# Kernel tuning notes

Hardware: AMD Instinct MI355X
Metric: run time of the kernel (lower is better)

The kernel has to match this reference:

```python
import jax, jax.numpy as jnp
import numpy as np

# ---- static config (mirrors init_kwargs) ----
EMBED_DIM = 128
NUM_HEADS = 4
N_SUB = 16       # token grid is N_SUB x N_SUB, seq = N_SUB**2
WINDOW = 4
SHIFT = 2
EPS = 1e-5
NEG_INF = -1e9


def _swin_mask(n_sub, ws, shift):
    """Standard Swin attention mask for shifted windows. [NW, T, T]."""
    img = np.zeros((n_sub, n_sub), np.int32)
    cnt = 0
    for hs in (slice(0, -ws), slice(-ws, -shift), slice(-shift, None)):
        for wsl in (slice(0, -ws), slice(-ws, -shift), slice(-shift, None)):
            img[hs, wsl] = cnt
            cnt += 1
    nw = n_sub // ws
    ids = img.reshape(nw, ws, nw, ws).transpose(0, 2, 1, 3).reshape(nw * nw, ws * ws)
    mask = np.where(ids[:, None, :] != ids[:, :, None], NEG_INF, 0.0).astype(np.float32)
    return jnp.asarray(mask)


MASK = _swin_mask(N_SUB, WINDOW, SHIFT)


def _inorm(v):
    # InstanceNorm2d (affine=False) over spatial dims, per (batch, seq, channel)
    m = v.mean(axis=(-2, -1), keepdims=True)
    var = v.var(axis=(-2, -1), keepdims=True)
    return (v - m) * jax.lax.rsqrt(var + EPS)


def _pw(x, w, b):
    # pointwise (1x1) linear over channel dim of [..., C, H, W]
    return jnp.einsum('...chw,cd->...dhw', x, w) + b[:, None, None]


def _window(x, nw, ws):
    # [B, n_sub, n_sub, C, H, W] -> [B, nw*nw, ws*ws, C, H, W]
    B = x.shape[0]
    C, H, W = x.shape[3:]
    x = x.reshape(B, nw, ws, nw, ws, C, H, W)
    return x.transpose(0, 1, 3, 2, 4, 5, 6, 7).reshape(B, nw * nw, ws * ws, C, H, W)


def _unwindow(x, nw, ws):
    B = x.shape[0]
    C, H, W = x.shape[3:]
    x = x.reshape(B, nw, nw, ws, ws, C, H, W)
    return x.transpose(0, 1, 3, 2, 4, 5, 6, 7).reshape(B, nw * ws, nw * ws, C, H, W)


def _swin_func_attn(v, w_q, b_q, w_k, b_k, w_v, b_v, w_o, b_o):
    B, S, C, H, W = v.shape
    nw = N_SUB // WINDOW
    g = v.reshape(B, N_SUB, N_SUB, C, H, W)
    if SHIFT > 0:
        g = jnp.roll(g, (-SHIFT, -SHIFT), axis=(1, 2))
    q = _window(_pw(g, w_q, b_q), nw, WINDOW)
    k = _window(_pw(g, w_k, b_k), nw, WINDOW)
    val = _window(_pw(g, w_v, b_v), nw, WINDOW)
    d = C // NUM_HEADS
    T = WINDOW * WINDOW
    split = lambda x: x.reshape(B, nw * nw, T, NUM_HEADS, d, H, W)
    q, k, val = split(q), split(k), split(val)
    # integral score: spatial mean of per-head dot products, scaled by sqrt(d)
    scale = 1.0 / (np.sqrt(d) * H * W)
    scores = jnp.einsum('bnthdxy,bnshdxy->bnhts', q, k) * scale
    scores = scores + MASK[None, :, None, :, :]
    attn = jax.nn.softmax(scores, axis=-1)
    o = jnp.einsum('bnhts,bnshdxy->bnthdxy', attn, val)
    o = o.reshape(B, nw * nw, T, C, H, W)
    o = _pw(o, w_o, b_o)
    o = _unwindow(o, nw, WINDOW)
    if SHIFT > 0:
        o = jnp.roll(o, (SHIFT, SHIFT), axis=(1, 2))
    return o.reshape(B, S, C, H, W)


def _mlp(x, w1, b1, w2, b2):
    return _pw(jax.nn.gelu(_pw(x, w1, b1)), w2, b2)


def setup_inputs() -> dict:
    key = jax.random.key(0)
    ks = jax.random.split(key, 8)
    B, S, C, H, W = 8, N_SUB * N_SUB, EMBED_DIM, 16, 16
    p = 0.02
    return {
        'v': jax.random.normal(ks[0], (B, S, C, H, W), jnp.float32),
        'w_q': jax.random.normal(ks[1], (C, C), jnp.float32) * p,
        'b_q': jnp.zeros((C,), jnp.float32),
        'w_k': jax.random.normal(ks[2], (C, C), jnp.float32) * p,
        'b_k': jnp.zeros((C,), jnp.float32),
        'w_v': jax.random.normal(ks[3], (C, C), jnp.float32) * p,
        'b_v': jnp.zeros((C,), jnp.float32),
        'w_o': jax.random.normal(ks[4], (C, C), jnp.float32) * p,
        'b_o': jnp.zeros((C,), jnp.float32),
        'w1': jax.random.normal(ks[5], (C, C), jnp.float32) * p,
        'b1': jnp.zeros((C,), jnp.float32),
        'w2': jax.random.normal(ks[6], (C, C), jnp.float32) * p,
        'b2': jnp.zeros((C,), jnp.float32),
    }


def reference(v, w_q, b_q, w_k, b_k, w_v, b_v, w_o, b_o, w1, b1, w2, b2):
    v = _swin_func_attn(_inorm(v), w_q, b_q, w_k, b_k, w_v, b_v, w_o, b_o) + v
    v = _mlp(_inorm(v), w1, b1, w2, b2) + v
    return v
```

## Files before the change

kernel.cpp:

```cpp
#include <hip/hip_runtime.h>
#include <cstdint>
#include <cstddef>

#define DI __device__ __forceinline__

typedef unsigned short u16;
typedef u16 u16x8 __attribute__((ext_vector_type(8)));
typedef u16 u16x4 __attribute__((ext_vector_type(4)));
typedef float f32x4 __attribute__((ext_vector_type(4)));
typedef __bf16 bf16x8 __attribute__((ext_vector_type(8)));

constexpr float EPSf  = 1e-5f;
constexpr float SCALE = 1.0f / (5.656854249492381f * 256.0f);

DI float bf2f(u16 u) { union { uint32_t i; float f; } v; v.i = ((uint32_t)u) << 16; return v.f; }
DI u16 f2bf(float f) {
    union { float f; uint32_t i; } v; v.f = f;
    uint32_t r = v.i + 0x7fffu + ((v.i >> 16) & 1u);
    return (u16)(r >> 16);
}

DI f32x4 MFMA(bf16x8 a, bf16x8 b, f32x4 c) {
    return __builtin_amdgcn_mfma_f32_16x16x32_bf16(a, b, c, 0, 0, 0);
}

DI int region3(int x) { return x < 12 ? 0 : (x < 14 ? 1 : 2); }

DI float gelu_f(float x) {
    float u = 1.5957691216f * x * (1.f + 0.044715f * x * x);
    return x * __builtin_amdgcn_rcpf(1.f + __expf(-u));
}

__global__ __launch_bounds__(256) void kw_prep(
        const float* __restrict__ w_q, const float* __restrict__ w_k,
        const float* __restrict__ w_v, const float* __restrict__ w_o,
        const float* __restrict__ w1,  const float* __restrict__ w2,
        u16* __restrict__ wt) {
    __shared__ float lds[128 * 129];
    const float* W;
    switch (blockIdx.x) {
        case 0: W = w_q; break; case 1: W = w_k; break; case 2: W = w_v; break;
        case 3: W = w_o; break; case 4: W = w1;  break; default: W = w2;  break;
    }
    u16* O = wt + blockIdx.x * 16384;
    int tid = threadIdx.x;
    for (int i = 0; i < 16; i++) {
        int flat = i * 1024 + tid * 4;
        float4 vv = *(const float4*)(W + flat);
        int c = flat >> 7, d = flat & 127;
        lds[c * 129 + d + 0] = vv.x; lds[c * 129 + d + 1] = vv.y;
        lds[c * 129 + d + 2] = vv.z; lds[c * 129 + d + 3] = vv.w;
    }
    __syncthreads();
    for (int i = 0; i < 32; i++) {
        int flat2 = i * 512 + tid * 2;
        int d = flat2 >> 7, c = flat2 & 127;
        u16 a = f2bf(lds[c * 129 + d]);
        u16 b = f2bf(lds[(c + 1) * 129 + d]);
        uint32_t pk = (uint32_t)a | ((uint32_t)b << 16);
        *(uint32_t*)(O + flat2) = pk;
    }
}

__global__ __launch_bounds__(512) void k2_qkv(
        const float* __restrict__ v, const u16* __restrict__ wt,
        const float* __restrict__ b_q, const float* __restrict__ b_k,
        const float* __restrict__ b_v,
        u16* __restrict__ Qg, u16* __restrict__ Kg, u16* __restrict__ Vg) {
    __shared__ u16 Abuf[256 * 136];
    __shared__ float red[2][4][128];
    __shared__ float stats[2][128];

    int tid = threadIdx.x;
    int wtk = blockIdx.x;
    int b = wtk >> 8, n = (wtk >> 4) & 15, t = wtk & 15;
    int wi = n >> 2, wj = n & 3, ti = t >> 2, tj = t & 3;
    int si = (wi * 4 + ti + 2) & 15, sj = (wj * 4 + tj + 2) & 15;
    const float* src = v + (size_t)(b * 256 + si * 16 + sj) * 32768;

    int xy = tid & 255, chh = tid >> 8;
    #pragma unroll 4
    for (int g = 0; g < 16; g++) {
        int c0 = chh * 64 + g * 4;
        float x0 = src[(c0 + 0) * 256 + xy];
        float x1 = src[(c0 + 1) * 256 + xy];
        float x2 = src[(c0 + 2) * 256 + xy];
        float x3 = src[(c0 + 3) * 256 + xy];
        u16x4 u; u.x = f2bf(x0); u.y = f2bf(x1); u.z = f2bf(x2); u.w = f2bf(x3);
        *(u16x4*)&Abuf[xy * 136 + c0] = u;
    }
    __syncthreads();
    {
        int c = tid & 127, p = tid >> 7;
        float s = 0.f, q = 0.f;
        for (int k = 0; k < 64; k++) {
            float x = bf2f(Abuf[(p * 64 + k) * 136 + c]);
            s += x; q += x * x;
        }
        red[0][p][c] = s; red[1][p][c] = q;
    }
    __syncthreads();
    if (tid < 128) {
        int c = tid;
        float s = red[0][0][c] + red[0][1][c] + red[0][2][c] + red[0][3][c];
        float q = red[1][0][c] + red[1][1][c] + red[1][2][c] + red[1][3][c];
        float mean = s * (1.f / 256.f);
        float var = q * (1.f / 256.f) - mean * mean;
        stats[0][c] = mean; stats[1][c] = rsqrtf(var + EPSf);
    }
    __syncthreads();
    for (int g = 0; g < 16; g++) {
        int c0 = chh * 64 + g * 4;
        u16x4 u = *(u16x4*)&Abuf[xy * 136 + c0];
        u.x = f2bf((bf2f(u.x) - stats[0][c0 + 0]) * stats[1][c0 + 0]);
        u.y = f2bf((bf2f(u.y) - stats[0][c0 + 1]) * stats[1][c0 + 1]);
        u.z = f2bf((bf2f(u.z) - stats[0][c0 + 2]) * stats[1][c0 + 2]);
        u.w = f2bf((bf2f(u.w) - stats[0][c0 + 3]) * stats[1][c0 + 3]);
        *(u16x4*)&Abuf[xy * 136 + c0] = u;
    }
    __syncthreads();

    int wave = tid >> 6, lane = tid & 63;
    int lrow = lane & 15, quad = lane >> 4;
    bf16x8 afr[2][4];
    for (int mi = 0; mi < 2; mi++) {
        int mt = wave * 2 + mi;
        for (int kt = 0; kt < 4; kt++)
            afr[mi][kt] = *(const bf16x8*)&Abuf[(mt * 16 + lrow) * 136 + kt * 32 + quad * 8];
    }
    __syncthreads();
    u16* WTs  = Abuf;
    u16* stgw = Abuf + 17408 + wave * 2176;
    for (int w = 0; w < 3; w++) {
        const u16* WTp = wt + w * 16384;
        const float* bias = (w == 0) ? b_q : (w == 1) ? b_k : b_v;
        u16* O = ((w == 0) ? Qg : (w == 1) ? Kg : Vg) + (size_t)wtk * 32768;
        if (w) __syncthreads();
        for (int i = 0; i < 4; i++) {
            int flat = i * 4096 + tid * 8;
            *(u16x8*)&WTs[(flat >> 7) * 136 + (flat & 127)] =
                *(const u16x8*)&WTp[flat];
        }
        __syncthreads();
        f32x4 acc[2][8];
        for (int mi = 0; mi < 2; mi++)
            for (int nt = 0; nt < 8; nt++) acc[mi][nt] = (f32x4){0.f, 0.f, 0.f, 0.f};
        for (int kt = 0; kt < 4; kt++) {
            for (int nt = 0; nt < 8; nt++) {
                bf16x8 bfr = *(const bf16x8*)&WTs[(nt * 16 + lrow) * 136 + kt * 32 + quad * 8];
                acc[0][nt] = MFMA(afr[0][kt], bfr, acc[0][nt]);
                acc[1][nt] = MFMA(afr[1][kt], bfr, acc[1][nt]);
            }
        }
        for (int mi = 0; mi < 2; mi++) {
            int mt = wave * 2 + mi;
            for (int nt = 0; nt < 8; nt++) {
                int d = nt * 16 + lrow;
                float bv = bias[d];
                for (int r = 0; r < 4; r++)
                    stgw[(quad * 4 + r) * 136 + d] = f2bf(acc[mi][nt][r] + bv);
            }
            for (int ro = 0; ro < 4; ro++) {
                int flat = ro * 512 + lane * 8;
                *(u16x8*)&O[mt * 2048 + flat] =
                    *(const u16x8*)&stgw[(flat >> 7) * 136 + (flat & 127)];
            }
        }
    }
}

__global__ __launch_bounds__(1024, 4) void k3_scores(
        const u16* __restrict__ Qg, const u16* __restrict__ Kg,
        float* __restrict__ spart) {
    __shared__ f32x4 red3[3][4][64];
    int tid = threadIdx.x;
    int bid = blockIdx.x;
    int b = bid >> 5, n = (bid >> 1) & 15, half = bid & 1;
    int wtb = (b * 16 + n) * 16;
    int lane = tid & 63, wave = tid >> 6;
    int head = wave & 3, sub = wave >> 2;
    int lrow = lane & 15, quad = lane >> 4;
    int xyb = half * 128 + sub * 32;
    const u16* Qp = Qg + (size_t)(wtb + lrow) * 32768 + (size_t)xyb * 128 + head * 32 + quad * 8;
    const u16* Kp = Kg + (size_t)(wtb + lrow) * 32768 + (size_t)xyb * 128 + head * 32 + quad * 8;
    f32x4 acc = {0.f, 0.f, 0.f, 0.f};
    #pragma unroll 4
    for (int kt = 0; kt < 32; kt++) {
        bf16x8 aq = *(const bf16x8*)(Qp + kt * 128);
        bf16x8 bk = *(const bf16x8*)(Kp + kt * 128);
        acc = MFMA(aq, bk, acc);
    }
    if (sub) red3[sub - 1][head][lane] = acc;
    __syncthreads();
    if (sub == 0) {
        f32x4 a0 = red3[0][head][lane];
        f32x4 a1 = red3[1][head][lane];
        f32x4 a2 = red3[2][head][lane];
        acc = acc + a0 + a1 + a2;
        float* sp = spart + (size_t)(((half * 8 + b) * 16 + n) * 4 + head) * 256;
        for (int r = 0; r < 4; r++) sp[(quad * 4 + r) * 16 + lrow] = acc[r];
    }
}

__global__ __launch_bounds__(512) void k4_attnout(
        const float* __restrict__ v, const u16* __restrict__ Vg,
        const float* __restrict__ spart, const u16* __restrict__ wt,
        const float* __restrict__ b_o, u16* __restrict__ v2) {
    __shared__ u16 Vc[32768];
    __shared__ u16 Obuf[256 * 136];
    __shared__ float attn[4][16][16];
    int tid = threadIdx.x;
    int bid = blockIdx.x;
    int b = bid >> 6, n = (bid >> 2) & 15, qtr = bid & 3;
    int wi = n >> 2, wj = n & 3;
    int wtb = (b * 16 + n) * 16;

    if (tid < 64) {
        int h = tid >> 4, t = tid & 15;
        int it = wi * 4 + (t >> 2) , jt = wj * 4 + (t & 3);
        int rt = region3(it) * 3 + region3(jt);
        const float* sp0 = spart + (size_t)(((0 + b) * 16 + n) * 4 + h) * 256 + t * 16;
        const float* sp1 = spart + (size_t)(((8 + b) * 16 + n) * 4 + h) * 256 + t * 16;
        float vals[16]; float mx = -1e30f;
        for (int s = 0; s < 16; s++) {
            int is = wi * 4 + (s >> 2), js = wj * 4 + (s & 3);
            int rs = region3(is) * 3 + region3(js);
            float sc = (sp0[s] + sp1[s]) * SCALE + (rs == rt ? 0.f : -1e9f);
            vals[s] = sc; mx = fmaxf(mx, sc);
        }
        float sum = 0.f;
        for (int s = 0; s < 16; s++) { vals[s] = __expf(vals[s] - mx); sum += vals[s]; }
        float inv = 1.f / sum;
        for (int s = 0; s < 16; s++) attn[h][t][s] = vals[s] * inv;
    }
    __syncthreads();

    int lane = tid & 63, wave = tid >> 6;
    int lrow = lane & 15, quad = lane >> 4;
    const u16* WoT = wt + 3 * 16384;

    for (int sub = 0; sub < 4; sub++) {
        int xyb = qtr * 64 + sub * 16;
        if (sub) __syncthreads();
        for (int it = 0; it < 8; it++) {
            int flat = (it * 512 + tid) * 8;
            int s = flat >> 11, rem = flat & 2047;
            *(u16x8*)&Vc[flat] =
                *(const u16x8*)&Vg[(size_t)(wtb + s) * 32768 + xyb * 128 + rem];
        }
        __syncthreads();
        {
            int c = tid & 127, xg = tid >> 7;
            int h = c >> 5;
            float vreg[4][16];
            for (int rep = 0; rep < 4; rep++) {
                int xyl = xg * 4 + rep;
                for (int s = 0; s < 16; s++)
                    vreg[rep][s] = bf2f(Vc[s * 2048 + xyl * 128 + c]);
            }
            for (int t = 0; t < 16; t++) {
                float oa0 = 0.f, oa1 = 0.f, oa2 = 0.f, oa3 = 0.f;
                for (int s = 0; s < 16; s++) {
                    float a = attn[h][t][s];
                    oa0 += a * vreg[0][s]; oa1 += a * vreg[1][s];
                    oa2 += a * vreg[2][s]; oa3 += a * vreg[3][s];
                }
                Obuf[(t * 16 + xg * 4 + 0) * 136 + c] = f2bf(oa0);
                Obuf[(t * 16 + xg * 4 + 1) * 136 + c] = f2bf(oa1);
                Obuf[(t * 16 + xg * 4 + 2) * 136 + c] = f2bf(oa2);
                Obuf[(t * 16 + xg * 4 + 3) * 136 + c] = f2bf(oa3);
            }
        }
        __syncthreads();
        bf16x8 afr[2][4];
        for (int mi = 0; mi < 2; mi++) {
            int mt = wave * 2 + mi;
            for (int kt = 0; kt < 4; kt++)
                afr[mi][kt] = *(const bf16x8*)&Obuf[(mt * 16 + lrow) * 136 + kt * 32 + quad * 8];
        }
        f32x4 acc[2][8];
        for (int mi = 0; mi < 2; mi++)
            for (int nt = 0; nt < 8; nt++) acc[mi][nt] = (f32x4){0.f, 0.f, 0.f, 0.f};
        for (int kt = 0; kt < 4; kt++) {
            for (int nt = 0; nt < 8; nt++) {
                bf16x8 bfr = *(const bf16x8*)&WoT[(nt * 16 + lrow) * 128 + kt * 32 + quad * 8];
                acc[0][nt] = MFMA(afr[0][kt], bfr, acc[0][nt]);
                acc[1][nt] = MFMA(afr[1][kt], bfr, acc[1][nt]);
            }
        }
        u16* stgw = Vc + wave * 2176;
        for (int mi = 0; mi < 2; mi++) {
            int mt = wave * 2 + mi;
            int sd = (((wi * 4 + (mt >> 2) + 2) & 15) << 4) | ((wj * 4 + (mt & 3) + 2) & 15);
            size_t tokbase = (size_t)(b * 256 + sd) * 32768;
            for (int nt = 0; nt < 8; nt++) {
                int c = nt * 16 + lrow;
                float bv = b_o[c];
                float4 res = *(const float4*)&v[tokbase + (size_t)c * 256 + xyb + quad * 4];
                stgw[(quad * 4 + 0) * 136 + c] = f2bf(acc[mi][nt][0] + bv + res.x);
                stgw[(quad * 4 + 1) * 136 + c] = f2bf(acc[mi][nt][1] + bv + res.y);
                stgw[(quad * 4 + 2) * 136 + c] = f2bf(acc[mi][nt][2] + bv + res.z);
                stgw[(quad * 4 + 3) * 136 + c] = f2bf(acc[mi][nt][3] + bv + res.w);
            }
            size_t obase = tokbase + (size_t)xyb * 128;
            for (int ro = 0; ro < 4; ro++) {
                int flat = ro * 512 + lane * 8;
                *(u16x8*)&v2[obase + flat] =
                    *(const u16x8*)&stgw[(flat >> 7) * 136 + (flat & 127)];
            }
        }
    }
}

__global__ __launch_bounds__(512) void k6_mlp(
        const u16* __restrict__ v2, const u16* __restrict__ wt,
        const float* __restrict__ b1, const float* __restrict__ b2,
        float* __restrict__ out) {
    __shared__ u16 Nbuf[256 * 136];
    __shared__ u16 Hbuf[256 * 136];
    __shared__ float red[2][4][128];
    __shared__ float stats[3][128];
    int tid = threadIdx.x;
    size_t tok = blockIdx.x;
    const u16* src = v2 + tok * 32768;

    for (int it = 0; it < 8; it++) {
        int flat = (it * 512 + tid) * 8;
        int xy = flat >> 7, c = flat & 127;
        *(u16x8*)&Nbuf[xy * 136 + c] = *(const u16x8*)&src[flat];
    }
    __syncthreads();
    {
        int c = tid & 127, p = tid >> 7;
        float s = 0.f, q = 0.f;
        for (int k = 0; k < 64; k++) {
            float x = bf2f(Nbuf[(p * 64 + k) * 136 + c]);
            s += x; q += x * x;
        }
        red[0][p][c] = s; red[1][p][c] = q;
    }
    __syncthreads();
    if (tid < 128) {
        int c = tid;
        float s = red[0][0][c] + red[0][1][c] + red[0][2][c] + red[0][3][c];
        float q = red[1][0][c] + red[1][1][c] + red[1][2][c] + red[1][3][c];
        float mean = s * (1.f / 256.f);
        float var = q * (1.f / 256.f) - mean * mean;
        float rstd = rsqrtf(var + EPSf);
        stats[0][c] = mean; stats[1][c] = rstd; stats[2][c] = (var + EPSf) * rstd;
    }
    __syncthreads();
    {
        int c0 = (tid & 31) * 4, xyB = tid >> 5;
        for (int g = 0; g < 16; g++) {
            int xy = g * 16 + xyB;
            u16x4 u = *(u16x4*)&Nbuf[xy * 136 + c0];
            u.x = f2bf((bf2f(u.x) - stats[0][c0 + 0]) * stats[1][c0 + 0]);
            u.y = f2bf((bf2f(u.y) - stats[0][c0 + 1]) * stats[1][c0 + 1]);
            u.z = f2bf((bf2f(u.z) - stats[0][c0 + 2]) * stats[1][c0 + 2]);
            u.w = f2bf((bf2f(u.w) - stats[0][c0 + 3]) * stats[1][c0 + 3]);
            *(u16x4*)&Nbuf[xy * 136 + c0] = u;
        }
    }
    {
        const u16* W1T = wt + 4 * 16384;
        for (int i = 0; i < 4; i++) {
            int flat = i * 4096 + tid * 8;
            *(u16x8*)&Hbuf[(flat >> 7) * 136 + (flat & 127)] = *(const u16x8*)&W1T[flat];
        }
    }
    __syncthreads();

    int wave = tid >> 6, lane = tid & 63;
    int lrow = lane & 15, quad = lane >> 4;
    const u16* W2T = wt + 5 * 16384;

    {
        bf16x8 afr[2][4];
        for (int mi = 0; mi < 2; mi++) {
            int mt = wave * 2 + mi;
            for (int kt = 0; kt < 4; kt++)
                afr[mi][kt] = *(const bf16x8*)&Nbuf[(mt * 16 + lrow) * 136 + kt * 32 + quad * 8];
        }
        f32x4 acc[2][8];
        for (int mi = 0; mi < 2; mi++)
            for (int nt = 0; nt < 8; nt++) acc[mi][nt] = (f32x4){0.f, 0.f, 0.f, 0.f};
        for (int kt = 0; kt < 4; kt++) {
            for (int nt = 0; nt < 8; nt++) {
                bf16x8 bfr = *(const bf16x8*)&Hbuf[(nt * 16 + lrow) * 136 + kt * 32 + quad * 8];
                acc[0][nt] = MFMA(afr[0][kt], bfr, acc[0][nt]);
                acc[1][nt] = MFMA(afr[1][kt], bfr, acc[1][nt]);
            }
        }
        __syncthreads();
        for (int mi = 0; mi < 2; mi++) {
            int mt = wave * 2 + mi;
            for (int nt = 0; nt < 8; nt++) {
                int c = nt * 16 + lrow;
                float bv = b1[c];
                for (int r = 0; r < 4; r++) {
                    float x = acc[mi][nt][r] + bv;
                    Hbuf[(mt * 16 + quad * 4 + r) * 136 + c] = f2bf(gelu_f(x));
                }
            }
        }
    }
    {
        bf16x8 afr[2][4];
        for (int mi = 0; mi < 2; mi++) {
            int mt = wave * 2 + mi;
            for (int kt = 0; kt < 4; kt++)
                afr[mi][kt] = *(const bf16x8*)&Hbuf[(mt * 16 + lrow) * 136 + kt * 32 + quad * 8];
        }
        f32x4 acc[2][8];
        for (int mi = 0; mi < 2; mi++)
            for (int nt = 0; nt < 8; nt++) acc[mi][nt] = (f32x4){0.f, 0.f, 0.f, 0.f};
        for (int kt = 0; kt < 4; kt++) {
            for (int nt = 0; nt < 8; nt++) {
                bf16x8 bfr = *(const bf16x8*)&W2T[(nt * 16 + lrow) * 128 + kt * 32 + quad * 8];
                acc[0][nt] = MFMA(afr[0][kt], bfr, acc[0][nt]);
                acc[1][nt] = MFMA(afr[1][kt], bfr, acc[1][nt]);
            }
        }
        for (int mi = 0; mi < 2; mi++) {
            int mt = wave * 2 + mi;
            for (int nt = 0; nt < 8; nt++) {
                int c = nt * 16 + lrow;
                float mean = stats[0][c], sd = stats[2][c], bv = b2[c];
                f32x4 o4;
                for (int r = 0; r < 4; r++) {
                    int m = mt * 16 + quad * 4 + r;
                    float n2v = bf2f(Nbuf[m * 136 + c]);
                    o4[r] = acc[mi][nt][r] + bv + n2v * sd + mean;
                }
                *(f32x4*)&out[tok * 32768 + (size_t)c * 256 + mt * 16 + quad * 4] = o4;
            }
        }
    }
}

extern "C" void kernel_launch(void* const* d_in, const int* in_sizes, int n_in,
                              void* d_out, int out_size, void* d_ws, size_t ws_size,
                              hipStream_t stream) {
    const float* v   = (const float*)d_in[0];
    const float* w_q = (const float*)d_in[1];
    const float* b_q = (const float*)d_in[2];
    const float* w_k = (const float*)d_in[3];
    const float* b_k = (const float*)d_in[4];
    const float* w_v = (const float*)d_in[5];
    const float* b_v = (const float*)d_in[6];
    const float* w_o = (const float*)d_in[7];
    const float* b_o = (const float*)d_in[8];
    const float* w1  = (const float*)d_in[9];
    const float* b1  = (const float*)d_in[10];
    const float* w2  = (const float*)d_in[11];
    const float* b2  = (const float*)d_in[12];

    u16*   wt    = (u16*)d_ws;
    float* spart = (float*)((char*)d_ws + 196608);
    u16*   Qg    = (u16*)((char*)d_ws + 1245184);
    u16*   v2    = Qg;
    u16*   Vg    = (u16*)d_out;
    u16*   Kg    = (u16*)d_out + 67108864;
    float* out   = (float*)d_out;

    kw_prep  <<<6,    256,  0, stream>>>(w_q, w_k, w_v, w_o, w1, w2, wt);
    k2_qkv   <<<2048, 512,  0, stream>>>(v, wt, b_q, b_k, b_v, Qg, Kg, Vg);
    k3_scores<<<256,  1024, 0, stream>>>(Qg, Kg, spart);
    k4_attnout<<<512, 512,  0, stream>>>(v, Vg, spart, wt, b_o, v2);
    k6_mlp   <<<2048, 512,  0, stream>>>(v2, wt, b1, b2, out);
}
```

Measured before the change: 1.042 ms.

## Double block size to 1024 threads in qkv, attnout and mlp kernels

Raises k2_qkv, k4_attnout and k6_mlp to 1024 threads so each wave owns one 16-row M tile instead of two. k2 now loads the input with float4 reads, computes the norm stats in registers and applies them as a single fmaf while transposing into LDS. k2 and k6 stop staging the weights in LDS and read the B fragments straight from global/L2. The aim is more waves in flight, fewer LDS passes and fewer barriers, at the cost of extra global weight reads and launch bounds that may force register spilling.

```diff
diff --git a/kernel.cpp b/kernel.cpp
--- a/kernel.cpp
+++ b/kernel.cpp
@@ -62,13 +62,13 @@
     }
 }
 
-__global__ __launch_bounds__(512) void k2_qkv(
+__global__ __launch_bounds__(1024, 4) void k2_qkv(
         const float* __restrict__ v, const u16* __restrict__ wt,
         const float* __restrict__ b_q, const float* __restrict__ b_k,
         const float* __restrict__ b_v,
         u16* __restrict__ Qg, u16* __restrict__ Kg, u16* __restrict__ Vg) {
-    __shared__ u16 Abuf[256 * 136];
-    __shared__ float red[2][4][128];
+    __shared__ __align__(16) u16 Abuf[256 * 136];
+    __shared__ float red[2][8][128];
     __shared__ float stats[2][128];
 
     int tid = threadIdx.x;
@@ -78,93 +78,72 @@
     int si = (wi * 4 + ti + 2) & 15, sj = (wj * 4 + tj + 2) & 15;
     const float* src = v + (size_t)(b * 256 + si * 16 + sj) * 32768;
 
-    int xy = tid & 255, chh = tid >> 8;
-    #pragma unroll 4
-    for (int g = 0; g < 16; g++) {
-        int c0 = chh * 64 + g * 4;
-        float x0 = src[(c0 + 0) * 256 + xy];
-        float x1 = src[(c0 + 1) * 256 + xy];
-        float x2 = src[(c0 + 2) * 256 + xy];
-        float x3 = src[(c0 + 3) * 256 + xy];
-        u16x4 u; u.x = f2bf(x0); u.y = f2bf(x1); u.z = f2bf(x2); u.w = f2bf(x3);
-        *(u16x4*)&Abuf[xy * 136 + c0] = u;
-    }
-    __syncthreads();
-    {
-        int c = tid & 127, p = tid >> 7;
-        float s = 0.f, q = 0.f;
-        for (int k = 0; k < 64; k++) {
-            float x = bf2f(Abuf[(p * 64 + k) * 136 + c]);
-            s += x; q += x * x;
-        }
-        red[0][p][c] = s; red[1][p][c] = q;
-    }
+    int c = tid & 127, xyq = tid >> 7;
+    float vals[32];
+    float s = 0.f, q = 0.f;
+    #pragma unroll
+    for (int g = 0; g < 8; g++) {
+        float4 f = *(const float4*)(src + c * 256 + g * 32 + xyq * 4);
+        vals[g * 4 + 0] = f.x; vals[g * 4 + 1] = f.y;
+        vals[g * 4 + 2] = f.z; vals[g * 4 + 3] = f.w;
+        s += f.x + f.y + f.z + f.w;
+        q += f.x * f.x + f.y * f.y + f.z * f.z + f.w * f.w;
+    }
+    red[0][xyq][c] = s; red[1][xyq][c] = q;
     __syncthreads();
     if (tid < 128) {
-        int c = tid;
-        float s = red[0][0][c] + red[0][1][c] + red[0][2][c] + red[0][3][c];
-        float q = red[1][0][c] + red[1][1][c] + red[1][2][c] + red[1][3][c];
-        float mean = s * (1.f / 256.f);
-        float var = q * (1.f / 256.f) - mean * mean;
-        stats[0][c] = mean; stats[1][c] = rsqrtf(var + EPSf);
-    }
-    __syncthreads();
-    for (int g = 0; g < 16; g++) {
-        int c0 = chh * 64 + g * 4;
-        u16x4 u = *(u16x4*)&Abuf[xy * 136 + c0];
-        u.x = f2bf((bf2f(u.x) - stats[0][c0 + 0]) * stats[1][c0 + 0]);
-        u.y = f2bf((bf2f(u.y) - stats[0][c0 + 1]) * stats[1][c0 + 1]);
-        u.z = f2bf((bf2f(u.z) - stats[0][c0 + 2]) * stats[1][c0 + 2]);
-        u.w = f2bf((bf2f(u.w) - stats[0][c0 + 3]) * stats[1][c0 + 3]);
-        *(u16x4*)&Abuf[xy * 136 + c0] = u;
-    }
+        float ss = 0.f, qq = 0.f;
+        #pragma unroll
+        for (int p = 0; p < 8; p++) { ss += red[0][p][tid]; qq += red[1][p][tid]; }
+        float mean = ss * (1.f / 256.f);
+        float var = qq * (1.f / 256.f) - mean * mean;
+        float a = rsqrtf(var + EPSf);
+        stats[0][tid] = a; stats[1][tid] = -mean * a;
+    }
+    __syncthreads();
+    float na = stats[0][c], nb = stats[1][c];
+    #pragma unroll
+    for (int g = 0; g < 8; g++)
+        #pragma unroll
+        for (int j = 0; j < 4; j++)
+            Abuf[(g * 32 + xyq * 4 + j) * 136 + c] = f2bf(fmaf(vals[g * 4 + j], na, nb));
     __syncthreads();
 
     int wave = tid >> 6, lane = tid & 63;
     int lrow = lane & 15, quad = lane >> 4;
-    bf16x8 afr[2][4];
-    for (int mi = 0; mi < 2; mi++) {
-        int mt = wave * 2 + mi;
-        for (int kt = 0; kt < 4; kt++)
-            afr[mi][kt] = *(const bf16x8*)&Abuf[(mt * 16 + lrow) * 136 + kt * 32 + quad * 8];
-    }
-    __syncthreads();
-    u16* WTs  = Abuf;
-    u16* stgw = Abuf + 17408 + wave * 2176;
+    bf16x8 afr[4];
+    #pragma unroll
+    for (int kt = 0; kt < 4; kt++)
+        afr[kt] = *(const bf16x8*)&Abuf[(wave * 16 + lrow) * 136 + kt * 32 + quad * 8];
+    u16* stgw = Abuf + wave * 2176;
     for (int w = 0; w < 3; w++) {
         const u16* WTp = wt + w * 16384;
         const float* bias = (w == 0) ? b_q : (w == 1) ? b_k : b_v;
         u16* O = ((w == 0) ? Qg : (w == 1) ? Kg : Vg) + (size_t)wtk * 32768;
-        if (w) __syncthreads();
-        for (int i = 0; i < 4; i++) {
-            int flat = i * 4096 + tid * 8;
-            *(u16x8*)&WTs[(flat >> 7) * 136 + (flat & 127)] =
-                *(const u16x8*)&WTp[flat];
-        }
-        __syncthreads();
-        f32x4 acc[2][8];
-        for (int mi = 0; mi < 2; mi++)
-            for (int nt = 0; nt < 8; nt++) acc[mi][nt] = (f32x4){0.f, 0.f, 0.f, 0.f};
+        f32x4 acc[8];
+        #pragma unroll
+        for (int nt = 0; nt < 8; nt++) acc[nt] = (f32x4){0.f, 0.f, 0.f, 0.f};
+        #pragma unroll
         for (int kt = 0; kt < 4; kt++) {
+            #pragma unroll
             for (int nt = 0; nt < 8; nt++) {
-                bf16x8 bfr = *(const bf16x8*)&WTs[(nt * 16 + lrow) * 136 + kt * 32 + quad * 8];
-                acc[0][nt] = MFMA(afr[0][kt], bfr, acc[0][nt]);
-                acc[1][nt] = MFMA(afr[1][kt], bfr, acc[1][nt]);
-            }
-        }
-        for (int mi = 0; mi < 2; mi++) {
-            int mt = wave * 2 + mi;
-            for (int nt = 0; nt < 8; nt++) {
-                int d = nt * 16 + lrow;
-                float bv = bias[d];
-                for (int r = 0; r < 4; r++)
-                    stgw[(quad * 4 + r) * 136 + d] = f2bf(acc[mi][nt][r] + bv);
-            }
-            for (int ro = 0; ro < 4; ro++) {
-                int flat = ro * 512 + lane * 8;
-                *(u16x8*)&O[mt * 2048 + flat] =
-                    *(const u16x8*)&stgw[(flat >> 7) * 136 + (flat & 127)];
-            }
+                bf16x8 bfr = *(const bf16x8*)&WTp[(nt * 16 + lrow) * 128 + kt * 32 + quad * 8];
+                acc[nt] = MFMA(afr[kt], bfr, acc[nt]);
+            }
+        }
+        #pragma unroll
+        for (int nt = 0; nt < 8; nt++) {
+            int d = nt * 16 + lrow;
+            float bv = bias[d];
+            #pragma unroll
+            for (int r = 0; r < 4; r++)
+                stgw[(quad * 4 + r) * 136 + d] = f2bf(acc[nt][r] + bv);
+        }
+        #pragma unroll
+        for (int ro = 0; ro < 4; ro++) {
+            int flat = ro * 512 + lane * 8;
+            *(u16x8*)&O[wave * 2048 + flat] =
+                *(const u16x8*)&stgw[(flat >> 7) * 136 + (flat & 127)];
         }
     }
 }
@@ -202,12 +181,12 @@
     }
 }
 
-__global__ __launch_bounds__(512) void k4_attnout(
+__global__ __launch_bounds__(1024, 4) void k4_attnout(
         const float* __restrict__ v, const u16* __restrict__ Vg,
         const float* __restrict__ spart, const u16* __restrict__ wt,
         const float* __restrict__ b_o, u16* __restrict__ v2) {
-    __shared__ u16 Vc[32768];
-    __shared__ u16 Obuf[256 * 136];
+    __shared__ __align__(16) u16 Vc[32768];
+    __shared__ __align__(16) u16 Obuf[256 * 136];
     __shared__ float attn[4][16][16];
     int tid = threadIdx.x;
     int bid = blockIdx.x;
@@ -242,8 +221,9 @@
     for (int sub = 0; sub < 4; sub++) {
         int xyb = qtr * 64 + sub * 16;
         if (sub) __syncthreads();
-        for (int it = 0; it < 8; it++) {
-            int flat = (it * 512 + tid) * 8;
+        #pragma unroll
+        for (int it = 0; it < 4; it++) {
+            int flat = (it * 1024 + tid) * 8;
             int s = flat >> 11, rem = flat & 2047;
             *(u16x8*)&Vc[flat] =
                 *(const u16x8*)&Vg[(size_t)(wtb + s) * 32768 + xyb * 128 + rem];
@@ -252,89 +232,92 @@
         {
             int c = tid & 127, xg = tid >> 7;
             int h = c >> 5;
-            float vreg[4][16];
-            for (int rep = 0; rep < 4; rep++) {
-                int xyl = xg * 4 + rep;
+            float vreg[2][16];
+            #pragma unroll
+            for (int rep = 0; rep < 2; rep++) {
+                int xyl = xg * 2 + rep;
+                #pragma unroll
                 for (int s = 0; s < 16; s++)
                     vreg[rep][s] = bf2f(Vc[s * 2048 + xyl * 128 + c]);
             }
+            #pragma unroll
             for (int t = 0; t < 16; t++) {
-                float oa0 = 0.f, oa1 = 0.f, oa2 = 0.f, oa3 = 0.f;
+                float oa0 = 0.f, oa1 = 0.f;
+                #pragma unroll
                 for (int s = 0; s < 16; s++) {
                     float a = attn[h][t][s];
                     oa0 += a * vreg[0][s]; oa1 += a * vreg[1][s];
-                    oa2 += a * vreg[2][s]; oa3 += a * vreg[3][s];
                 }
-                Obuf[(t * 16 + xg * 4 + 0) * 136 + c] = f2bf(oa0);
-                Obuf[(t * 16 + xg * 4 + 1) * 136 + c] = f2bf(oa1);
-                Obuf[(t * 16 + xg * 4 + 2) * 136 + c] = f2bf(oa2);
-                Obuf[(t * 16 + xg * 4 + 3) * 136 + c] = f2bf(oa3);
+                Obuf[(t * 16 + xg * 2 + 0) * 136 + c] = f2bf(oa0);
+                Obuf[(t * 16 + xg * 2 + 1) * 136 + c] = f2bf(oa1);
             }
         }
         __syncthreads();
-        bf16x8 afr[2][4];
-        for (int mi = 0; mi < 2; mi++) {
-            int mt = wave * 2 + mi;
-            for (int kt = 0; kt < 4; kt++)
-                afr[mi][kt] = *(const bf16x8*)&Obuf[(mt * 16 + lrow) * 136 + kt * 32 + quad * 8];
-        }
-        f32x4 acc[2][8];
-        for (int mi = 0; mi < 2; mi++)
-            for (int nt = 0; nt < 8; nt++) acc[mi][nt] = (f32x4){0.f, 0.f, 0.f, 0.f};
+        bf16x8 afr[4];
+        #pragma unroll
+        for (int kt = 0; kt < 4; kt++)
+            afr[kt] = *(const bf16x8*)&Obuf[(wave * 16 + lrow) * 136 + kt * 32 + quad * 8];
+        f32x4 acc[8];
+        #pragma unroll
+        for (int nt = 0; nt < 8; nt++) acc[nt] = (f32x4){0.f, 0.f, 0.f, 0.f};
+        #pragma unroll
         for (int kt = 0; kt < 4; kt++) {
+            #pragma unroll
             for (int nt = 0; nt < 8; nt++) {
                 bf16x8 bfr = *(const bf16x8*)&WoT[(nt * 16 + lrow) * 128 + kt * 32 + quad * 8];
-                acc[0][nt] = MFMA(afr[0][kt], bfr, acc[0][nt]);
-                acc[1][nt] = MFMA(afr[1][kt], bfr, acc[1][nt]);
-            }
-        }
-        u16* stgw = Vc + wave * 2176;
-        for (int mi = 0; mi < 2; mi++) {
-            int mt = wave * 2 + mi;
-            int sd = (((wi * 4 + (mt >> 2) + 2) & 15) << 4) | ((wj * 4 + (mt & 3) + 2) & 15);
-            size_t tokbase = (size_t)(b * 256 + sd) * 32768;
-            for (int nt = 0; nt < 8; nt++) {
-                int c = nt * 16 + lrow;
-                float bv = b_o[c];
-                float4 res = *(const float4*)&v[tokbase + (size_t)c * 256 + xyb + quad * 4];
-                stgw[(quad * 4 + 0) * 136 + c] = f2bf(acc[mi][nt][0] + bv + res.x);
-                stgw[(quad * 4 + 1) * 136 + c] = f2bf(acc[mi][nt][1] + bv + res.y);
-                stgw[(quad * 4 + 2) * 136 + c] = f2bf(acc[mi][nt][2] + bv + res.z);
-                stgw[(quad * 4 + 3) * 136 + c] = f2bf(acc[mi][nt][3] + bv + res.w);
-            }
-            size_t obase = tokbase + (size_t)xyb * 128;
-            for (int ro = 0; ro < 4; ro++) {
-                int flat = ro * 512 + lane * 8;
-                *(u16x8*)&v2[obase + flat] =
-                    *(const u16x8*)&stgw[(flat >> 7) * 136 + (flat & 127)];
-            }
-        }
-    }
-}
-
-__global__ __launch_bounds__(512) void k6_mlp(
+                acc[nt] = MFMA(afr[kt], bfr, acc[nt]);
+            }
+        }
+        int mt = wave;
+        int sd = (((wi * 4 + (mt >> 2) + 2) & 15) << 4) | ((wj * 4 + (mt & 3) + 2) & 15);
+        size_t tokbase = (size_t)(b * 256 + sd) * 32768;
+        u16* stgw = Obuf + wave * 2176;
+        #pragma unroll
+        for (int nt = 0; nt < 8; nt++) {
+            int cc = nt * 16 + lrow;
+            float bv = b_o[cc];
+            float4 res = *(const float4*)&v[tokbase + (size_t)cc * 256 + xyb + quad * 4];
+            stgw[(quad * 4 + 0) * 136 + cc] = f2bf(acc[nt][0] + bv + res.x);
+            stgw[(quad * 4 + 1) * 136 + cc] = f2bf(acc[nt][1] + bv + res.y);
+            stgw[(quad * 4 + 2) * 136 + cc] = f2bf(acc[nt][2] + bv + res.z);
+            stgw[(quad * 4 + 3) * 136 + cc] = f2bf(acc[nt][3] + bv + res.w);
+        }
+        size_t obase = tokbase + (size_t)xyb * 128;
+        #pragma unroll
+        for (int ro = 0; ro < 4; ro++) {
+            int flat = ro * 512 + lane * 8;
+            *(u16x8*)&v2[obase + flat] =
+                *(const u16x8*)&stgw[(flat >> 7) * 136 + (flat & 127)];
+        }
+    }
+}
+
+__global__ __launch_bounds__(1024, 4) void k6_mlp(
         const u16* __restrict__ v2, const u16* __restrict__ wt,
         const float* __restrict__ b1, const float* __restrict__ b2,
         float* __restrict__ out) {
-    __shared__ u16 Nbuf[256 * 136];
-    __shared__ u16 Hbuf[256 * 136];
-    __shared__ float red[2][4][128];
+    __shared__ __align__(16) u16 Nbuf[256 * 136];
+    __shared__ __align__(16) u16 Hbuf[256 * 136];
+    __shared__ float red[2][8][128];
     __shared__ float stats[3][128];
     int tid = threadIdx.x;
     size_t tok = blockIdx.x;
     const u16* src = v2 + tok * 32768;
 
-    for (int it = 0; it < 8; it++) {
-        int flat = (it * 512 + tid) * 8;
-        int xy = flat >> 7, c = flat & 127;
-        *(u16x8*)&Nbuf[xy * 136 + c] = *(const u16x8*)&src[flat];
+    u16x8 ld[4];
+    #pragma unroll
+    for (int it = 0; it < 4; it++) {
+        int flat = (it * 1024 + tid) * 8;
+        int xy = flat >> 7, cc = flat & 127;
+        ld[it] = *(const u16x8*)&src[flat];
+        *(u16x8*)&Nbuf[xy * 136 + cc] = ld[it];
     }
     __syncthreads();
     {
         int c = tid & 127, p = tid >> 7;
         float s = 0.f, q = 0.f;
-        for (int k = 0; k < 64; k++) {
-            float x = bf2f(Nbuf[(p * 64 + k) * 136 + c]);
+        for (int k = 0; k < 32; k++) {
+            float x = bf2f(Nbuf[(p * 32 + k) * 136 + c]);
             s += x; q += x * x;
         }
         red[0][p][c] = s; red[1][p][c] = q;
@@ -342,8 +325,9 @@
     __syncthreads();
     if (tid < 128) {
         int c = tid;
-        float s = red[0][0][c] + red[0][1][c] + red[0][2][c] + red[0][3][c];
-        float q = red[1][0][c] + red[1][1][c] + red[1][2][c] + red[1][3][c];
+        float s = 0.f, q = 0.f;
+        #pragma unroll
+        for (int p = 0; p < 8; p++) { s += red[0][p][c]; q += red[1][p][c]; }
         float mean = s * (1.f / 256.f);
         float var = q * (1.f / 256.f) - mean * mean;
         float rstd = rsqrtf(var + EPSf);
@@ -351,90 +335,87 @@
     }
     __syncthreads();
     {
-        int c0 = (tid & 31) * 4, xyB = tid >> 5;
-        for (int g = 0; g < 16; g++) {
-            int xy = g * 16 + xyB;
-            u16x4 u = *(u16x4*)&Nbuf[xy * 136 + c0];
-            u.x = f2bf((bf2f(u.x) - stats[0][c0 + 0]) * stats[1][c0 + 0]);
-            u.y = f2bf((bf2f(u.y) - stats[0][c0 + 1]) * stats[1][c0 + 1]);
-            u.z = f2bf((bf2f(u.z) - stats[0][c0 + 2]) * stats[1][c0 + 2]);
-            u.w = f2bf((bf2f(u.w) - stats[0][c0 + 3]) * stats[1][c0 + 3]);
-            *(u16x4*)&Nbuf[xy * 136 + c0] = u;
-        }
-    }
-    {
-        const u16* W1T = wt + 4 * 16384;
-        for (int i = 0; i < 4; i++) {
-            int flat = i * 4096 + tid * 8;
-            *(u16x8*)&Hbuf[(flat >> 7) * 136 + (flat & 127)] = *(const u16x8*)&W1T[flat];
+        int c0 = (tid & 15) * 8;
+        float a[8], bb[8];
+        #pragma unroll
+        for (int j = 0; j < 8; j++) {
+            float m = stats[0][c0 + j], r = stats[1][c0 + j];
+            a[j] = r; bb[j] = -m * r;
+        }
+        #pragma unroll
+        for (int it = 0; it < 4; it++) {
+            int flat = (it * 1024 + tid) * 8;
+            int xy = flat >> 7;
+            u16x8 u = ld[it];
+            u16x8 o;
+            #pragma unroll
+            for (int j = 0; j < 8; j++)
+                o[j] = f2bf(fmaf(bf2f(u[j]), a[j], bb[j]));
+            *(u16x8*)&Nbuf[xy * 136 + c0] = o;
         }
     }
     __syncthreads();
 
     int wave = tid >> 6, lane = tid & 63;
     int lrow = lane & 15, quad = lane >> 4;
+    const u16* W1T = wt + 4 * 16384;
     const u16* W2T = wt + 5 * 16384;
 
     {
-        bf16x8 afr[2][4];
-        for (int mi = 0; mi < 2; mi++) {
-            int mt = wave * 2 + mi;
-            for (int kt = 0; kt < 4; kt++)
-                afr[mi][kt] = *(const bf16x8*)&Nbuf[(mt * 16 + lrow) * 136 + kt * 32 + quad * 8];
-        }
-        f32x4 acc[2][8];
-        for (int mi = 0; mi < 2; mi++)
-            for (int nt = 0; nt < 8; nt++) acc[mi][nt] = (f32x4){0.f, 0.f, 0.f, 0.f};
+        bf16x8 afr[4];
+        #pragma unroll
+        for (int kt = 0; kt < 4; kt++)
+            afr[kt] = *(const bf16x8*)&Nbuf[(wave * 16 + lrow) * 136 + kt * 32 + quad * 8];
+        f32x4 acc[8];
+        #pragma unroll
+        for (int nt = 0; nt < 8; nt++) acc[nt] = (f32x4){0.f, 0.f, 0.f, 0.f};
+        #pragma unroll
         for (int kt = 0; kt < 4; kt++) {
+            #pragma unroll
             for (int nt = 0; nt < 8; nt++) {
-                bf16x8 bfr = *(const bf16x8*)&Hbuf[(nt * 16 + lrow) * 136 + kt * 32 + quad * 8];
-                acc[0][nt] = MFMA(afr[0][kt], bfr, acc[0][nt]);
-                acc[1][nt] = MFMA(afr[1][kt], bfr, acc[1][nt]);
-            }
-        }
-        __syncthreads();
-        for (int mi = 0; mi < 2; mi++) {
-            int mt = wave * 2 + mi;
-            for (int nt = 0; nt < 8; nt++) {
-                int c = nt * 16 + lrow;
-                float bv = b1[c];
-                for (int r = 0; r < 4; r++) {
-                    float x = acc[mi][nt][r] + bv;
-                    Hbuf[(mt * 16 + quad * 4 + r) * 136 + c] = f2bf(gelu_f(x));
-                }
+                bf16x8 bfr = *(const bf16x8*)&W1T[(nt * 16 + lrow) * 128 + kt * 32 + quad * 8];
+                acc[nt] = MFMA(afr[kt], bfr, acc[nt]);
+            }
+        }
+        #pragma unroll
+        for (int nt = 0; nt < 8; nt++) {
+            int c = nt * 16 + lrow;
+            float bv = b1[c];
+            #pragma unroll
+            for (int r = 0; r < 4; r++) {
+                float x = acc[nt][r] + bv;
+                Hbuf[(wave * 16 + quad * 4 + r) * 136 + c] = f2bf(gelu_f(x));
             }
         }
     }
     {
-        bf16x8 afr[2][4];
-        for (int mi = 0; mi < 2; mi++) {
-            int mt = wave * 2 + mi;
-            for (int kt = 0; kt < 4; kt++)
-                afr[mi][kt] = *(const bf16x8*)&Hbuf[(mt * 16 + lrow) * 136 + kt * 32 + quad * 8];
-        }
-        f32x4 acc[2][8];
-        for (int mi = 0; mi < 2; mi++)
-            for (int nt = 0; nt < 8; nt++) acc[mi][nt] = (f32x4){0.f, 0.f, 0.f, 0.f};
+        bf16x8 afr[4];
+        #pragma unroll
+        for (int kt = 0; kt < 4; kt++)
+            afr[kt] = *(const bf16x8*)&Hbuf[(wave * 16 + lrow) * 136 + kt * 32 + quad * 8];
+        f32x4 acc[8];
+        #pragma unroll
+        for (int nt = 0; nt < 8; nt++) acc[nt] = (f32x4){0.f, 0.f, 0.f, 0.f};
+        #pragma unroll
         for (int kt = 0; kt < 4; kt++) {
+            #pragma unroll
             for (int nt = 0; nt < 8; nt++) {
                 bf16x8 bfr = *(const bf16x8*)&W2T[(nt * 16 + lrow) * 128 + kt * 32 + quad * 8];
-                acc[0][nt] = MFMA(afr[0][kt], bfr, acc[0][nt]);
-                acc[1][nt] = MFMA(afr[1][kt], bfr, acc[1][nt]);
-            }
-        }
-        for (int mi = 0; mi < 2; mi++) {
-            int mt = wave * 2 + mi;
-            for (int nt = 0; nt < 8; nt++) {
-                int c = nt * 16 + lrow;
-                float mean = stats[0][c], sd = stats[2][c], bv = b2[c];
-                f32x4 o4;
-                for (int r = 0; r < 4; r++) {
-                    int m = mt * 16 + quad * 4 + r;
-                    float n2v = bf2f(Nbuf[m * 136 + c]);
-                    o4[r] = acc[mi][nt][r] + bv + n2v * sd + mean;
-                }
-                *(f32x4*)&out[tok * 32768 + (size_t)c * 256 + mt * 16 + quad * 4] = o4;
-            }
+                acc[nt] = MFMA(afr[kt], bfr, acc[nt]);
+            }
+        }
+        #pragma unroll
+        for (int nt = 0; nt < 8; nt++) {
+            int c = nt * 16 + lrow;
+            float mean = stats[0][c], sd = stats[2][c], bv = b2[c];
+            f32x4 o4;
+            #pragma unroll
+            for (int r = 0; r < 4; r++) {
+                int m = wave * 16 + quad * 4 + r;
+                float n2v = bf2f(Nbuf[m * 136 + c]);
+                o4[r] = acc[nt][r] + bv + n2v * sd + mean;
+            }
+            *(f32x4*)&out[tok * 32768 + (size_t)c * 256 + wave * 16 + quad * 4] = o4;
         }
     }
 }
@@ -465,8 +446,8 @@
     float* out   = (float*)d_out;
 
     kw_prep  <<<6,    256,  0, stream>>>(w_q, w_k, w_v, w_o, w1, w2, wt);
-    k2_qkv   <<<2048, 512,  0, stream>>>(v, wt, b_q, b_k, b_v, Qg, Kg, Vg);
+    k2_qkv   <<<2048, 1024, 0, stream>>>(v, wt, b_q, b_k, b_v, Qg, Kg, Vg);
     k3_scores<<<256,  1024, 0, stream>>>(Qg, Kg, spart);
-    k4_attnout<<<512, 512,  0, stream>>>(v, Vg, spart, wt, b_o, v2);
-    k6_mlp   <<<2048, 512,  0, stream>>>(v2, wt, b1, b2, out);
-}
+    k4_attnout<<<512, 1024, 0, stream>>>(v, Vg, spart, wt, b_o, v2);
+    k6_mlp   <<<2048, 1024, 0, stream>>>(v2, wt, b1, b2, out);
+}
```

Result: slower. 1.510 ms (+45.0%).
